# Optimization experiments

Measured on AMD Instinct MI355X. Metric: run time of the kernel, lower is better.

The kernel has to match this reference:

```python
import jax, jax.numpy as jnp
import numpy as np

TOP_K = 2
CAPACITY_FACTOR = 1.0


def _ffn(x, w1, w2):
    # SwiGLU FFN: x [N, D], w1 [D, 2F], w2 [F, D]
    h = x @ w1
    x1, x2 = jnp.split(h, 2, axis=-1)
    return (x1 * jax.nn.silu(x2)) @ w2


def setup_inputs() -> dict:
    key = jax.random.key(0)
    ks = jax.random.split(key, 6)
    B, S, D, F, E_r, E_s = 4, 2048, 2048, 1024, 7, 1
    sc_in = 1.0 / np.sqrt(D)
    sc_mid = 1.0 / np.sqrt(F)
    return {
        "x": jax.random.normal(ks[0], (B, S, D), dtype=jnp.float32),
        "gate_w": jax.random.normal(ks[1], (D, E_r), dtype=jnp.float32) * sc_in,
        "expert_bias": jnp.zeros((E_r,), dtype=jnp.float32),
        "shared_w1": jax.random.normal(ks[2], (E_s, D, 2 * F), dtype=jnp.float32) * sc_in,
        "shared_w2": jax.random.normal(ks[3], (E_s, F, D), dtype=jnp.float32) * sc_mid,
        "routed_w1": jax.random.normal(ks[4], (E_r, D, 2 * F), dtype=jnp.float32) * sc_in,
        "routed_w2": jax.random.normal(ks[5], (E_r, F, D), dtype=jnp.float32) * sc_mid,
    }


def reference(x, gate_w, expert_bias, shared_w1, shared_w2, routed_w1, routed_w2):
    B, S, D = x.shape
    E_r = gate_w.shape[1]
    T = B * S
    capacity = max(1, int(CAPACITY_FACTOR * T / E_r))
    flat_x = x.reshape(T, D)

    # shared experts: applied to every token, summed
    shared_sum = jax.vmap(_ffn, in_axes=(None, 0, 0))(flat_x, shared_w1, shared_w2).sum(0)

    # gating (eval mode: no noise, no dropout)
    gate_logits = flat_x @ gate_w + expert_bias  # [T, E_r]
    aff = jax.nn.sigmoid(gate_logits)
    _, topk_idx = jax.lax.top_k(aff, TOP_K)  # [T, K]
    # mask[t, e] = expert e is among token t's top-k
    mask = (topk_idx[:, :, None] == jnp.arange(E_r)[None, None, :]).any(axis=1)  # [T, E_r]

    # per-expert capacity selection: keep top-`capacity` masked tokens by affinity
    score = jnp.where(mask, aff, -1.0).T  # [E_r, T]; aff >= 0 so -1 sorts last
    _, sel_idx = jax.lax.top_k(score, capacity)  # [E_r, capacity] token ids
    kept = jnp.take_along_axis(mask.T, sel_idx, axis=1)  # [E_r, cap]
    w = jnp.where(kept, jnp.take_along_axis(aff.T, sel_idx, axis=1), 0.0)  # [E_r, cap]

    # grouped gather -> FFN -> weighted scatter-add
    inp = flat_x[sel_idx]  # [E_r, cap, D]
    out = jax.vmap(_ffn)(inp, routed_w1, routed_w2)  # [E_r, cap, D]
    routed_sum = jnp.zeros_like(flat_x).at[sel_idx].add(out * w[:, :, None])

    return (shared_sum + routed_sum).reshape(B, S, D)
```

## Files before the change

### kernel.cpp

```cpp
#include <hip/hip_runtime.h>
#include <hip/hip_bf16.h>

typedef unsigned long long u64;
typedef __bf16 bf16x8 __attribute__((ext_vector_type(8)));
typedef float f32x4 __attribute__((ext_vector_type(4)));
typedef unsigned short ushort8_t __attribute__((ext_vector_type(8)));

#define TOKS 8192
#define DMODEL 2048
#define FD 1024
#define NEXP 7
#define CAP 1170
#define CAPP 1280
#define URT256 67
#define URT128 134

#define MFMA16(a, b, c) __builtin_amdgcn_mfma_f32_16x16x32_bf16(a, b, c, 0, 0, 0)

__device__ __forceinline__ unsigned short f2bf(float f) {
  __hip_bfloat16 b = __float2bfloat16(f);
  return __builtin_bit_cast(unsigned short, b);
}
__device__ __forceinline__ float bf2f(unsigned short u) {
  __hip_bfloat16 b = __builtin_bit_cast(__hip_bfloat16, u);
  return __bfloat162float(b);
}
__device__ __forceinline__ void gload_lds16(const void* g, void* l) {
  __builtin_amdgcn_global_load_lds(
      (const __attribute__((address_space(1))) void*)g,
      (__attribute__((address_space(3))) void*)l, 16, 0, 0);
}

__global__ __launch_bounds__(256) void k_conv_gate(
    const float* __restrict__ x, const float* __restrict__ gw,
    const float* __restrict__ bias, unsigned short* __restrict__ xb,
    u64* __restrict__ keys) {
  const int t = blockIdx.x;
  const int tid = threadIdx.x;
  const int lane = tid & 63, wv = tid >> 6;
  const float* xr = x + (long)t * DMODEL;
  const int i0 = tid * 8;
  float4 v0 = *(const float4*)&xr[i0];
  float4 v1 = *(const float4*)&xr[i0 + 4];
  float xv[8] = {v0.x, v0.y, v0.z, v0.w, v1.x, v1.y, v1.z, v1.w};
  ushort8_t o;
#pragma unroll
  for (int j = 0; j < 8; ++j) o[j] = f2bf(xv[j]);
  *(ushort8_t*)&xb[(long)t * DMODEL + i0] = o;
  double acc[NEXP];
#pragma unroll
  for (int e = 0; e < NEXP; ++e) acc[e] = 0.0;
#pragma unroll
  for (int j = 0; j < 8; ++j) {
    const float* g = gw + (long)(i0 + j) * NEXP;
    double xd = (double)xv[j];
#pragma unroll
    for (int e = 0; e < NEXP; ++e) acc[e] += xd * (double)g[e];
  }
#pragma unroll
  for (int e = 0; e < NEXP; ++e)
    for (int off = 32; off > 0; off >>= 1)
      acc[e] += __shfl_down(acc[e], off, 64);
  __shared__ double red[4][NEXP];
  if (lane == 0)
#pragma unroll
    for (int e = 0; e < NEXP; ++e) red[wv][e] = acc[e];
  __syncthreads();
  if (tid == 0) {
    float aff[NEXP];
#pragma unroll
    for (int e = 0; e < NEXP; ++e) {
      double lg = red[0][e] + red[1][e] + red[2][e] + red[3][e] + (double)bias[e];
      aff[e] = (float)(1.0 / (1.0 + exp(-lg)));
    }
    int i1 = 0;
    for (int e = 1; e < NEXP; ++e) if (aff[e] > aff[i1]) i1 = e;
    int i2 = -1;
    for (int e = 0; e < NEXP; ++e) {
      if (e == i1) continue;
      if (i2 < 0 || aff[e] > aff[i2]) i2 = e;
    }
#pragma unroll
    for (int e = 0; e < NEXP; ++e) {
      u64 key = (u64)(0xFFFFFFFFu - (unsigned)t);
      if (e == i1 || e == i2) key |= ((u64)__float_as_uint(aff[e])) << 32;
      keys[(long)e * TOKS + t] = key;
    }
  }
}

template <bool PERM>
__global__ __launch_bounds__(256) void k_tr64(
    const float* __restrict__ in0, const float* __restrict__ inr,
    unsigned short* __restrict__ out, int R, int C) {
  __shared__ float t[64][65];
  const int z = blockIdx.z;
  const float* in = (z == 0) ? in0 : (inr + (long)(z - 1) * R * C);
  unsigned short* o = out + (long)z * R * C;
  const int c0 = blockIdx.x * 64;
  const int r0 = blockIdx.y * 64;
  const int tid = threadIdx.x;
  const int rr = tid >> 4;
  const int cc4 = (tid & 15) * 4;
#pragma unroll
  for (int i = 0; i < 4; ++i) {
    int r = rr + 16 * i;
    float4 v = *(const float4*)&in[(long)(r0 + r) * C + c0 + cc4];
    t[r][cc4 + 0] = v.x;
    t[r][cc4 + 1] = v.y;
    t[r][cc4 + 2] = v.z;
    t[r][cc4 + 3] = v.w;
  }
  __syncthreads();
#pragma unroll
  for (int h = 0; h < 2; ++h) {
    int c = tid + h * 256;
    int oc = c >> 3;
    int j = c & 7;
    ushort8_t v8;
#pragma unroll
    for (int q = 0; q < 8; ++q) v8[q] = f2bf(t[j * 8 + q][oc]);
    int gc = c0 + oc;
    long orow = PERM ? (long)(((gc & 1023) >> 4) * 32 + ((gc >> 10) << 4) + (gc & 15))
                     : (long)gc;
    *(ushort8_t*)&o[orow * R + r0 + j * 8] = v8;
  }
}

__global__ __launch_bounds__(1024) void k_select(
    const u64* __restrict__ keys, int* __restrict__ sel,
    float* __restrict__ selw, unsigned* __restrict__ cnt,
    int* __restrict__ inv) {
  __shared__ unsigned hist[256];
  __shared__ u64 s_prefix;
  __shared__ unsigned s_k;
  __shared__ unsigned s_cnt;
  const int e = blockIdx.x;
  const u64* kk = keys + (long)e * TOKS;
  const int tid = threadIdx.x;
  if (tid == 0) { s_prefix = 0; s_k = CAP; s_cnt = 0; }
  __syncthreads();
  for (int shift = 56; shift >= 0; shift -= 8) {
    if (tid < 256) hist[tid] = 0;
    __syncthreads();
    u64 pref = s_prefix;
    for (int i = tid; i < TOKS; i += 1024) {
      u64 key = kk[i];
      bool match = (shift == 56) || ((key >> (shift + 8)) == pref);
      if (match) atomicAdd(&hist[(unsigned)(key >> shift) & 255u], 1u);
    }
    __syncthreads();
    if (tid == 0) {
      unsigned k = s_k, cum = 0;
      for (int b = 255; b >= 0; --b) {
        unsigned c = hist[b];
        if (cum + c >= k) {
          s_prefix = (s_prefix << 8) | (unsigned)b;
          s_k = k - cum;
          break;
        }
        cum += c;
      }
    }
    __syncthreads();
  }
  const u64 T = s_prefix;
  for (int i = tid; i < TOKS; i += 1024) {
    u64 key = kk[i];
    if (key >= T) {
      unsigned p = atomicAdd(&s_cnt, 1u);
      int tok = (int)(0xFFFFFFFFu - (unsigned)(key & 0xFFFFFFFFull));
      unsigned vb = (unsigned)(key >> 32);
      sel[e * CAPP + p] = tok;
      selw[e * CAPP + p] = vb ? __uint_as_float(vb) : 0.0f;
      if (vb) {
        unsigned pos = atomicAdd(&cnt[tok], 1u);
        inv[tok * 2 + pos] = e * CAPP + (int)p;
      }
    }
  }
  for (int i = CAP + tid; i < CAPP; i += 1024) {
    sel[e * CAPP + i] = 0;
    selw[e * CAPP + i] = 0.0f;
  }
}

__global__ __launch_bounds__(256) void k_combine(
    float* __restrict__ out, const unsigned short* __restrict__ o_all,
    const int* __restrict__ inv, const unsigned* __restrict__ cnt) {
  const int tok = blockIdx.x;
  const unsigned c = cnt[tok];
  int i0 = -1, i1 = -1;
  if (c > 0) {
    i0 = inv[tok * 2];
    if (c > 1) {
      i1 = inv[tok * 2 + 1];
      if (i1 < i0) { int t = i0; i0 = i1; i1 = t; }
    }
  }
  const int col = threadIdx.x * 8;
  ushort8_t s = *(const ushort8_t*)&o_all[(long)tok * DMODEL + col];
  float v[8];
#pragma unroll
  for (int q = 0; q < 8; ++q) v[q] = bf2f(s[q]);
  if (i0 >= 0) {
    ushort8_t r = *(const ushort8_t*)&o_all[(long)(TOKS + i0) * DMODEL + col];
#pragma unroll
    for (int q = 0; q < 8; ++q) v[q] += bf2f(r[q]);
  }
  if (i1 >= 0) {
    ushort8_t r = *(const ushort8_t*)&o_all[(long)(TOKS + i1) * DMODEL + col];
#pragma unroll
    for (int q = 0; q < 8; ++q) v[q] += bf2f(r[q]);
  }
  float* op = out + (long)tok * DMODEL + col;
  *(float4*)op = make_float4(v[0], v[1], v[2], v[3]);
  *(float4*)(op + 4) = make_float4(v[4], v[5], v[6], v[7]);
}

__global__ __launch_bounds__(512, 2) void k_g1(
    const unsigned short* __restrict__ Abase,
    const unsigned short* __restrict__ Wbase,
    unsigned short* __restrict__ a_all, const int* __restrict__ sel) {
  constexpr int K = DMODEL;
  constexpr int N = 2048;
  constexpr int nk = K >> 6;
  extern __shared__ unsigned short lds[];
  const int tid = threadIdx.x;
  const int w = tid >> 6;
  const int lane = tid & 63;

  const int bx = blockIdx.x;
  const int by_u = blockIdx.y;

  int e, zw, m0l;
  if (by_u < 32) { e = -1; zw = 0; m0l = by_u << 8; }
  else { int q = by_u - 32; e = q / 5; zw = e + 1; m0l = (q % 5) << 8; }
  const long crow0_u = (e < 0) ? (long)m0l : (8192 + (long)e * CAPP + m0l);
  const long n0 = (long)bx * 256;
  const unsigned short* Bm = Wbase + (long)zw * N * K;

  const int wr = w >> 2;
  const int wc = w & 3;
  const int lr = lane & 15;
  const int kq = lane >> 4;

  const unsigned short* aP[2][2];
  const unsigned short* bP[2][2];
  int dstOff[2];
#pragma unroll
  for (int j = 0; j < 2; ++j) {
    int L = w * 128 + j * 64 + lane;
    int r = L >> 3;
    int cEl = ((L & 7) * 8) ^ ((r & 7) * 8);
    dstOff[j] = (w * 2 + j) * 512;
#pragma unroll
    for (int h = 0; h < 2; ++h) {
      long ar = (e < 0) ? (long)(m0l + h * 128 + r)
                        : (long)sel[e * CAPP + m0l + h * 128 + r];
      aP[h][j] = Abase + ar * (long)K + cEl;
      bP[h][j] = Bm + (n0 + h * 128 + r) * (long)K + cEl;
    }
  }

  auto STAGE = [&](int seg, int d, int ts) {
    unsigned short* base = lds + ((d << 2) + seg) * 8192;
    const unsigned short *p0, *p1;
    if (seg < 2) { p0 = aP[seg][0]; p1 = aP[seg][1]; }
    else         { p0 = bP[seg - 2][0]; p1 = bP[seg - 2][1]; }
    long ko = (long)ts * 64;
    gload_lds16(p0 + ko, base + dstOff[0]);
    gload_lds16(p1 + ko, base + dstOff[1]);
  };

  const int aSegT = wr;
  const int bSegT = 2 + (wc >> 1);
  const int colSw0 = (kq * 8) ^ ((lr & 7) * 8);
  const int colSw1 = (32 + kq * 8) ^ ((lr & 7) * 8);
  const int bRow = (wc & 1) * 64 + lr;

  STAGE(0, 0, 0); STAGE(1, 0, 0); STAGE(2, 0, 0); STAGE(3, 0, 0);
  STAGE(0, 1, 1); STAGE(1, 1, 1);
  asm volatile("s_waitcnt vmcnt(4)" ::: "memory");
  __builtin_amdgcn_sched_barrier(0);
  __builtin_amdgcn_s_barrier();
  __builtin_amdgcn_sched_barrier(0);

  f32x4 acc[8][4] = {};

#pragma unroll 1
  for (int T = 0; T < nk; ++T) {
    const int d = T & 1, dn = d ^ 1;
    int t1 = T + 1; if (t1 >= nk) t1 -= nk;
    int t2 = T + 2; if (t2 >= nk) t2 -= nk;
    const unsigned short* aSeg = lds + ((d << 2) + aSegT) * 8192;
    const unsigned short* bSeg = lds + ((d << 2) + bSegT) * 8192;
    bf16x8 af[8], b0, b1;

#pragma unroll
    for (int m = 0; m < 8; ++m)
      af[m] = *(const bf16x8*)&aSeg[(m * 16 + lr) * 64 + colSw0];
    b0 = *(const bf16x8*)&bSeg[(bRow + 0) * 64 + colSw0];
    b1 = *(const bf16x8*)&bSeg[(bRow + 16) * 64 + colSw0];
    __builtin_amdgcn_sched_barrier(0);
    STAGE(2, dn, t1);
    __builtin_amdgcn_sched_barrier(0);
    __builtin_amdgcn_s_barrier();
    asm volatile("s_waitcnt lgkmcnt(0)" ::: "memory");
    __builtin_amdgcn_sched_barrier(0);
    __builtin_amdgcn_s_setprio(1);
#pragma unroll
    for (int m = 0; m < 8; ++m) {
      acc[m][0] = MFMA16(af[m], b0, acc[m][0]);
      acc[m][1] = MFMA16(af[m], b1, acc[m][1]);
    }
    __builtin_amdgcn_s_setprio(0);
    __builtin_amdgcn_sched_barrier(0);
    __builtin_amdgcn_s_barrier();
    __builtin_amdgcn_sched_barrier(0);

    b0 = *(const bf16x8*)&bSeg[(bRow + 32) * 64 + colSw0];
    b1 = *(const bf16x8*)&bSeg[(bRow + 48) * 64 + colSw0];
    __builtin_amdgcn_sched_barrier(0);
    STAGE(3, dn, t1);
    __builtin_amdgcn_sched_barrier(0);
    __builtin_amdgcn_s_barrier();
    asm volatile("s_waitcnt lgkmcnt(0)" ::: "memory");
    __builtin_amdgcn_sched_barrier(0);
    __builtin_amdgcn_s_setprio(1);
#pragma unroll
    for (int m = 0; m < 8; ++m) {
      acc[m][2] = MFMA16(af[m], b0, acc[m][2]);
      acc[m][3] = MFMA16(af[m], b1, acc[m][3]);
    }
    __builtin_amdgcn_s_setprio(0);
    __builtin_amdgcn_sched_barrier(0);
    __builtin_amdgcn_s_barrier();
    __builtin_amdgcn_sched_barrier(0);

#pragma unroll
    for (int m = 0; m < 8; ++m)
      af[m] = *(const bf16x8*)&aSeg[(m * 16 + lr) * 64 + colSw1];
    b0 = *(const bf16x8*)&bSeg[(bRow + 0) * 64 + colSw1];
    b1 = *(const bf16x8*)&bSeg[(bRow + 16) * 64 + colSw1];
    __builtin_amdgcn_sched_barrier(0);
    __builtin_amdgcn_s_barrier();
    asm volatile("s_waitcnt lgkmcnt(0)" ::: "memory");
    __builtin_amdgcn_sched_barrier(0);
    __builtin_amdgcn_s_setprio(1);
#pragma unroll
    for (int m = 0; m < 8; ++m) {
      acc[m][0] = MFMA16(af[m], b0, acc[m][0]);
      acc[m][1] = MFMA16(af[m], b1, acc[m][1]);
    }
    __builtin_amdgcn_s_setprio(0);
    __builtin_amdgcn_sched_barrier(0);
    __builtin_amdgcn_s_barrier();
    __builtin_amdgcn_sched_barrier(0);

    b0 = *(const bf16x8*)&bSeg[(bRow + 32) * 64 + colSw1];
    b1 = *(const bf16x8*)&bSeg[(bRow + 48) * 64 + colSw1];
    __builtin_amdgcn_sched_barrier(0);
    STAGE(0, d, t2);
    STAGE(1, d, t2);
    asm volatile("s_waitcnt vmcnt(4)" ::: "memory");
    __builtin_amdgcn_sched_barrier(0);
    __builtin_amdgcn_s_barrier();
    asm volatile("s_waitcnt lgkmcnt(0)" ::: "memory");
    __builtin_amdgcn_sched_barrier(0);
    __builtin_amdgcn_s_setprio(1);
#pragma unroll
    for (int m = 0; m < 8; ++m) {
      acc[m][2] = MFMA16(af[m], b0, acc[m][2]);
      acc[m][3] = MFMA16(af[m], b1, acc[m][3]);
    }
    __builtin_amdgcn_s_setprio(0);
    __builtin_amdgcn_sched_barrier(0);
    __builtin_amdgcn_s_barrier();
    __builtin_amdgcn_sched_barrier(0);
  }
  asm volatile("s_waitcnt vmcnt(0)" ::: "memory");

  const int r0q = (lane >> 4) * 4;
  const int cc = lane & 15;
  const long gcol0 = (n0 >> 1) + wc * 32;
#pragma unroll
  for (int m = 0; m < 8; ++m)
#pragma unroll
    for (int rj = 0; rj < 4; ++rj) {
      long row = crow0_u + wr * 128 + m * 16 + r0q + rj;
#pragma unroll
      for (int q2 = 0; q2 < 2; ++q2) {
        float x1v = acc[m][2 * q2][rj];
        float x2v = acc[m][2 * q2 + 1][rj];
        float s = x2v / (1.0f + __expf(-x2v));
        a_all[row * FD + gcol0 + q2 * 16 + cc] = f2bf(x1v * s);
      }
    }
}

__global__ __launch_bounds__(512, 4) void k_g2(
    const unsigned short* __restrict__ Abase,
    const unsigned short* __restrict__ Wbase,
    unsigned short* __restrict__ o_all, const float* __restrict__ selw) {
  constexpr int K = FD;
  constexpr int N = DMODEL;
  constexpr int nk = K >> 5;
  __shared__ unsigned short lds[2][8192];
  const int tid = threadIdx.x & 255;
  const int isUpper = 0;
  (void)isUpper;
  const int w = tid >> 6;
  const int lane = tid & 63;

  int lin = blockIdx.x + ((int)blockIdx.y << 4);
  int gt = (lin & 7) * 268 + (lin >> 3);
  int ct, rt, su;
  if (gt < 2048) { su = gt >> 7; int rr = gt & 127; ct = rr >> 3; rt = rr & 7; }
  else           { su = 16;      int rr = gt - 2048; ct = rr / 6; rt = rr % 6; }
  const int by_u = su * 8 + rt;
  const int bx = ct;

  int e, zw, m0l;
  if (by_u < 64) { e = -1; zw = 0; m0l = by_u << 7; }
  else { int q = by_u - 64; e = q / 10; zw = e + 1; m0l = (q % 10) << 7; }
  const long crow0_u = (e < 0) ? (long)m0l : (8192 + (long)e * CAPP + m0l);
  const long n0 = (long)bx * 128;
  const unsigned short* Bm = Wbase + (long)zw * N * K;

  const int r_ = (w << 4) + (lane >> 2);
  const int p_ = lane & 3;
  const unsigned short* aSrc[2];
  const unsigned short* bSrc[2];
#pragma unroll
  for (int c = 0; c < 2; ++c) {
    int rsg = c * 64 + r_;
    int q = p_ ^ ((rsg >> 1) & 3);
    aSrc[c] = Abase + (crow0_u + rsg) * (long)K + q * 8;
    bSrc[c] = Bm + (n0 + rsg) * (long)K + q * 8;
  }
  const int dst0 = tid * 8;

  auto STAGE = [&](int buf, int kt) {
    const long ko = (long)kt * 32;
#pragma unroll
    for (int c = 0; c < 2; ++c) {
      gload_lds16(aSrc[c] + ko, &lds[buf][c * 2048 + dst0]);
      gload_lds16(bSrc[c] + ko, &lds[buf][4096 + c * 2048 + dst0]);
    }
  };

  const int wr = w >> 1, wc = w & 1;
  const int lr = lane & 15, kq = lane >> 4;
  const int slot = (kq ^ ((lr >> 1) & 3)) * 8;
  const int aRow = wr * 64 + lr;
  const int bRow = wc * 64 + lr;

  STAGE(0, 0);
  asm volatile("s_waitcnt vmcnt(0)" ::: "memory");
  __builtin_amdgcn_sched_barrier(0);
  __builtin_amdgcn_s_barrier();
  __builtin_amdgcn_sched_barrier(0);

  f32x4 acc[4][4] = {};
  int cur = 0;

#pragma unroll 1
  for (int kt = 0; kt < nk; ++kt) {
    if (kt + 1 < nk) STAGE(cur ^ 1, kt + 1);
    const unsigned short* aSeg = &lds[cur][0];
    const unsigned short* bSeg = &lds[cur][4096];
    bf16x8 af[4], bf[4];
#pragma unroll
    for (int m = 0; m < 4; ++m)
      af[m] = *(const bf16x8*)&aSeg[(aRow + m * 16) * 32 + slot];
#pragma unroll
    for (int n = 0; n < 4; ++n)
      bf[n] = *(const bf16x8*)&bSeg[(bRow + n * 16) * 32 + slot];
    asm volatile("s_waitcnt lgkmcnt(0)" ::: "memory");
    __builtin_amdgcn_sched_barrier(0);
    __builtin_amdgcn_s_setprio(1);
#pragma unroll
    for (int m = 0; m < 4; ++m)
#pragma unroll
      for (int n = 0; n < 4; ++n)
        acc[m][n] = MFMA16(af[m], bf[n], acc[m][n]);
    __builtin_amdgcn_s_setprio(0);
    asm volatile("s_waitcnt vmcnt(0)" ::: "memory");
    __builtin_amdgcn_sched_barrier(0);
    __builtin_amdgcn_s_barrier();
    __builtin_amdgcn_sched_barrier(0);
    cur ^= 1;
  }

  const int r0q = (lane >> 4) * 4;
  const int cc = lane & 15;
  const long ccol0 = n0 + wc * 64;
#pragma unroll
  for (int m = 0; m < 4; ++m)
#pragma unroll
    for (int rj = 0; rj < 4; ++rj) {
      int lrow = m0l + wr * 64 + m * 16 + r0q + rj;
      float wgt = (e < 0) ? 1.0f : selw[e * CAPP + (lrow - m0l) + (m0l)];
      long row = crow0_u + wr * 64 + m * 16 + r0q + rj;
#pragma unroll
      for (int n = 0; n < 4; ++n)
        o_all[row * DMODEL + ccol0 + n * 16 + cc] = f2bf(acc[m][n][rj] * wgt);
    }
}

extern "C" void kernel_launch(void* const* d_in, const int* in_sizes, int n_in,
                              void* d_out, int out_size, void* d_ws,
                              size_t ws_size, hipStream_t stream) {
  (void)in_sizes; (void)n_in; (void)out_size; (void)ws_size;
  const float* x = (const float*)d_in[0];
  const float* gw = (const float*)d_in[1];
  const float* eb = (const float*)d_in[2];
  const float* sw1 = (const float*)d_in[3];
  const float* sw2 = (const float*)d_in[4];
  const float* rw1 = (const float*)d_in[5];
  const float* rw2 = (const float*)d_in[6];
  float* out = (float*)d_out;

  char* ws = (char*)d_ws;
  size_t off = 0;
  auto alloc = [&](size_t bytes) {
    size_t o = off;
    off += (bytes + 255) & ~(size_t)255;
    return o;
  };
  unsigned short* xb    = (unsigned short*)(ws + alloc((size_t)TOKS * DMODEL * 2));
  unsigned short* w1t   = (unsigned short*)(ws + alloc((size_t)8 * DMODEL * (2 * FD) * 2));
  unsigned short* w2t   = (unsigned short*)(ws + alloc((size_t)8 * DMODEL * FD * 2));
  unsigned short* a_all = (unsigned short*)(ws + alloc((size_t)(TOKS + NEXP * CAPP) * FD * 2));
  unsigned short* o_all = (unsigned short*)(ws + alloc((size_t)(TOKS + NEXP * CAPP) * DMODEL * 2));
  u64* keys = (u64*)(ws + alloc((size_t)NEXP * TOKS * 8));
  int* sel  = (int*)(ws + alloc((size_t)NEXP * CAPP * 4));
  float* selw = (float*)(ws + alloc((size_t)NEXP * CAPP * 4));
  unsigned* cnt = (unsigned*)(ws + alloc((size_t)TOKS * 4));
  int* inv = (int*)(ws + alloc((size_t)TOKS * 2 * 4));

  const size_t LDSB = 131072;

  k_conv_gate<<<TOKS, 256, 0, stream>>>(x, gw, eb, xb, keys);
  k_tr64<true><<<dim3(32, 32, 8), 256, 0, stream>>>(sw1, rw1, w1t, DMODEL, 2 * FD);
  k_tr64<false><<<dim3(32, 16, 8), 256, 0, stream>>>(sw2, rw2, w2t, FD, DMODEL);
  hipMemsetAsync(cnt, 0, (size_t)TOKS * 4, stream);
  k_select<<<NEXP, 1024, 0, stream>>>(keys, sel, selw, cnt, inv);
  k_g1<<<dim3(8, URT256), 512, LDSB, stream>>>(xb, w1t, a_all, sel);
  k_g2<<<dim3(16, URT128), 256, 0, stream>>>(a_all, w2t, o_all, selw);
  k_combine<<<TOKS, 256, 0, stream>>>(out, o_all, inv, cnt);
}
```

Before: 496.5 us.

## Reuse 256x256 pipelined GEMM kernel for second MoE projection and fold count reset

Drops the separate 128x128 double-buffered down-projection kernel and runs the second GEMM through the templated 256x256, 512-thread pipelined kernel used for the first projection, with WHICH selecting K, the A-row source and the epilogue. The aim is higher operand reuse per block and the more tuned LDS pipeline. The counter reset moves from a hipMemsetAsync into the gate kernel, which removes one stream operation. The larger tiles give fewer blocks (8x67) and may lower occupancy or balance, and the down projection has only K=1024.

```diff
diff --git a/kernel.cpp b/kernel.cpp
--- a/kernel.cpp
+++ b/kernel.cpp
@@ -13,7 +13,6 @@
 #define CAP 1170
 #define CAPP 1280
 #define URT256 67
-#define URT128 134
 
 #define MFMA16(a, b, c) __builtin_amdgcn_mfma_f32_16x16x32_bf16(a, b, c, 0, 0, 0)
 
@@ -34,10 +33,11 @@
 __global__ __launch_bounds__(256) void k_conv_gate(
     const float* __restrict__ x, const float* __restrict__ gw,
     const float* __restrict__ bias, unsigned short* __restrict__ xb,
-    u64* __restrict__ keys) {
+    u64* __restrict__ keys, unsigned* __restrict__ cnt) {
   const int t = blockIdx.x;
   const int tid = threadIdx.x;
   const int lane = tid & 63, wv = tid >> 6;
+  if (tid == 0) cnt[t] = 0;
   const float* xr = x + (long)t * DMODEL;
   const int i0 = tid * 8;
   float4 v0 = *(const float4*)&xr[i0];
@@ -218,11 +218,13 @@
   *(float4*)(op + 4) = make_float4(v[4], v[5], v[6], v[7]);
 }
 
-__global__ __launch_bounds__(512, 2) void k_g1(
+template <int WHICH>
+__global__ __launch_bounds__(512, 2) void k_moe(
     const unsigned short* __restrict__ Abase,
     const unsigned short* __restrict__ Wbase,
-    unsigned short* __restrict__ a_all, const int* __restrict__ sel) {
-  constexpr int K = DMODEL;
+    unsigned short* __restrict__ obuf, const int* __restrict__ sel,
+    const float* __restrict__ selw) {
+  constexpr int K = (WHICH == 1) ? DMODEL : FD;
   constexpr int N = 2048;
   constexpr int nk = K >> 6;
   extern __shared__ unsigned short lds[];
@@ -256,8 +258,12 @@
     dstOff[j] = (w * 2 + j) * 512;
 #pragma unroll
     for (int h = 0; h < 2; ++h) {
-      long ar = (e < 0) ? (long)(m0l + h * 128 + r)
-                        : (long)sel[e * CAPP + m0l + h * 128 + r];
+      long ar;
+      if (WHICH == 1)
+        ar = (e < 0) ? (long)(m0l + h * 128 + r)
+                     : (long)sel[e * CAPP + m0l + h * 128 + r];
+      else
+        ar = crow0_u + h * 128 + r;
       aP[h][j] = Abase + ar * (long)K + cEl;
       bP[h][j] = Bm + (n0 + h * 128 + r) * (long)K + cEl;
     }
@@ -383,130 +389,36 @@
 
   const int r0q = (lane >> 4) * 4;
   const int cc = lane & 15;
-  const long gcol0 = (n0 >> 1) + wc * 32;
-#pragma unroll
-  for (int m = 0; m < 8; ++m)
-#pragma unroll
-    for (int rj = 0; rj < 4; ++rj) {
-      long row = crow0_u + wr * 128 + m * 16 + r0q + rj;
-#pragma unroll
-      for (int q2 = 0; q2 < 2; ++q2) {
-        float x1v = acc[m][2 * q2][rj];
-        float x2v = acc[m][2 * q2 + 1][rj];
-        float s = x2v / (1.0f + __expf(-x2v));
-        a_all[row * FD + gcol0 + q2 * 16 + cc] = f2bf(x1v * s);
+
+  if (WHICH == 1) {
+    const long gcol0 = (n0 >> 1) + wc * 32;
+#pragma unroll
+    for (int m = 0; m < 8; ++m)
+#pragma unroll
+      for (int rj = 0; rj < 4; ++rj) {
+        long row = crow0_u + wr * 128 + m * 16 + r0q + rj;
+#pragma unroll
+        for (int q2 = 0; q2 < 2; ++q2) {
+          float x1v = acc[m][2 * q2][rj];
+          float x2v = acc[m][2 * q2 + 1][rj];
+          float s = x2v / (1.0f + __expf(-x2v));
+          obuf[row * FD + gcol0 + q2 * 16 + cc] = f2bf(x1v * s);
+        }
       }
-    }
-}
-
-__global__ __launch_bounds__(512, 4) void k_g2(
-    const unsigned short* __restrict__ Abase,
-    const unsigned short* __restrict__ Wbase,
-    unsigned short* __restrict__ o_all, const float* __restrict__ selw) {
-  constexpr int K = FD;
-  constexpr int N = DMODEL;
-  constexpr int nk = K >> 5;
-  __shared__ unsigned short lds[2][8192];
-  const int tid = threadIdx.x & 255;
-  const int isUpper = 0;
-  (void)isUpper;
-  const int w = tid >> 6;
-  const int lane = tid & 63;
-
-  int lin = blockIdx.x + ((int)blockIdx.y << 4);
-  int gt = (lin & 7) * 268 + (lin >> 3);
-  int ct, rt, su;
-  if (gt < 2048) { su = gt >> 7; int rr = gt & 127; ct = rr >> 3; rt = rr & 7; }
-  else           { su = 16;      int rr = gt - 2048; ct = rr / 6; rt = rr % 6; }
-  const int by_u = su * 8 + rt;
-  const int bx = ct;
-
-  int e, zw, m0l;
-  if (by_u < 64) { e = -1; zw = 0; m0l = by_u << 7; }
-  else { int q = by_u - 64; e = q / 10; zw = e + 1; m0l = (q % 10) << 7; }
-  const long crow0_u = (e < 0) ? (long)m0l : (8192 + (long)e * CAPP + m0l);
-  const long n0 = (long)bx * 128;
-  const unsigned short* Bm = Wbase + (long)zw * N * K;
-
-  const int r_ = (w << 4) + (lane >> 2);
-  const int p_ = lane & 3;
-  const unsigned short* aSrc[2];
-  const unsigned short* bSrc[2];
-#pragma unroll
-  for (int c = 0; c < 2; ++c) {
-    int rsg = c * 64 + r_;
-    int q = p_ ^ ((rsg >> 1) & 3);
-    aSrc[c] = Abase + (crow0_u + rsg) * (long)K + q * 8;
-    bSrc[c] = Bm + (n0 + rsg) * (long)K + q * 8;
-  }
-  const int dst0 = tid * 8;
-
-  auto STAGE = [&](int buf, int kt) {
-    const long ko = (long)kt * 32;
-#pragma unroll
-    for (int c = 0; c < 2; ++c) {
-      gload_lds16(aSrc[c] + ko, &lds[buf][c * 2048 + dst0]);
-      gload_lds16(bSrc[c] + ko, &lds[buf][4096 + c * 2048 + dst0]);
-    }
-  };
-
-  const int wr = w >> 1, wc = w & 1;
-  const int lr = lane & 15, kq = lane >> 4;
-  const int slot = (kq ^ ((lr >> 1) & 3)) * 8;
-  const int aRow = wr * 64 + lr;
-  const int bRow = wc * 64 + lr;
-
-  STAGE(0, 0);
-  asm volatile("s_waitcnt vmcnt(0)" ::: "memory");
-  __builtin_amdgcn_sched_barrier(0);
-  __builtin_amdgcn_s_barrier();
-  __builtin_amdgcn_sched_barrier(0);
-
-  f32x4 acc[4][4] = {};
-  int cur = 0;
-
-#pragma unroll 1
-  for (int kt = 0; kt < nk; ++kt) {
-    if (kt + 1 < nk) STAGE(cur ^ 1, kt + 1);
-    const unsigned short* aSeg = &lds[cur][0];
-    const unsigned short* bSeg = &lds[cur][4096];
-    bf16x8 af[4], bf[4];
-#pragma unroll
-    for (int m = 0; m < 4; ++m)
-      af[m] = *(const bf16x8*)&aSeg[(aRow + m * 16) * 32 + slot];
-#pragma unroll
-    for (int n = 0; n < 4; ++n)
-      bf[n] = *(const bf16x8*)&bSeg[(bRow + n * 16) * 32 + slot];
-    asm volatile("s_waitcnt lgkmcnt(0)" ::: "memory");
-    __builtin_amdgcn_sched_barrier(0);
-    __builtin_amdgcn_s_setprio(1);
-#pragma unroll
-    for (int m = 0; m < 4; ++m)
-#pragma unroll
-      for (int n = 0; n < 4; ++n)
-        acc[m][n] = MFMA16(af[m], bf[n], acc[m][n]);
-    __builtin_amdgcn_s_setprio(0);
-    asm volatile("s_waitcnt vmcnt(0)" ::: "memory");
-    __builtin_amdgcn_sched_barrier(0);
-    __builtin_amdgcn_s_barrier();
-    __builtin_amdgcn_sched_barrier(0);
-    cur ^= 1;
-  }
-
-  const int r0q = (lane >> 4) * 4;
-  const int cc = lane & 15;
-  const long ccol0 = n0 + wc * 64;
-#pragma unroll
-  for (int m = 0; m < 4; ++m)
-#pragma unroll
-    for (int rj = 0; rj < 4; ++rj) {
-      int lrow = m0l + wr * 64 + m * 16 + r0q + rj;
-      float wgt = (e < 0) ? 1.0f : selw[e * CAPP + (lrow - m0l) + (m0l)];
-      long row = crow0_u + wr * 64 + m * 16 + r0q + rj;
-#pragma unroll
-      for (int n = 0; n < 4; ++n)
-        o_all[row * DMODEL + ccol0 + n * 16 + cc] = f2bf(acc[m][n][rj] * wgt);
-    }
+  } else {
+    const long ccol0 = n0 + wc * 64;
+#pragma unroll
+    for (int m = 0; m < 8; ++m)
+#pragma unroll
+      for (int rj = 0; rj < 4; ++rj) {
+        int lrow = m0l + wr * 128 + m * 16 + r0q + rj;
+        float wgt = (e < 0) ? 1.0f : selw[e * CAPP + lrow];
+        long row = crow0_u + wr * 128 + m * 16 + r0q + rj;
+#pragma unroll
+        for (int n = 0; n < 4; ++n)
+          obuf[row * DMODEL + ccol0 + n * 16 + cc] = f2bf(acc[m][n][rj] * wgt);
+      }
+  }
 }
 
 extern "C" void kernel_launch(void* const* d_in, const int* in_sizes, int n_in,
@@ -542,12 +454,11 @@
 
   const size_t LDSB = 131072;
 
-  k_conv_gate<<<TOKS, 256, 0, stream>>>(x, gw, eb, xb, keys);
+  k_conv_gate<<<TOKS, 256, 0, stream>>>(x, gw, eb, xb, keys, cnt);
   k_tr64<true><<<dim3(32, 32, 8), 256, 0, stream>>>(sw1, rw1, w1t, DMODEL, 2 * FD);
   k_tr64<false><<<dim3(32, 16, 8), 256, 0, stream>>>(sw2, rw2, w2t, FD, DMODEL);
-  hipMemsetAsync(cnt, 0, (size_t)TOKS * 4, stream);
   k_select<<<NEXP, 1024, 0, stream>>>(keys, sel, selw, cnt, inv);
-  k_g1<<<dim3(8, URT256), 512, LDSB, stream>>>(xb, w1t, a_all, sel);
-  k_g2<<<dim3(16, URT128), 256, 0, stream>>>(a_all, w2t, o_all, selw);
+  k_moe<1><<<dim3(8, URT256), 512, LDSB, stream>>>(xb, w1t, a_all, sel, nullptr);
+  k_moe<2><<<dim3(8, URT256), 512, LDSB, stream>>>(a_all, w2t, o_all, nullptr, selw);
   k_combine<<<TOKS, 256, 0, stream>>>(out, o_all, inv, cnt);
 }
```

After: 512.1 us. 1.03x slower.
